# Kernel tuning notes

Measured on AMD Instinct MI355X. Metric: run time of the kernel, lower is better.

The kernel has to match this reference:

```python
import jax, jax.numpy as jnp
import numpy as np

TOP_K = 5  # top_k edges kept per node row


def _edge_update(x, w0, w1, w2, wo, bo):
    # x: [B, N, D] -> masked dense adjacency [B, N, N]
    B, N, D = x.shape
    # pairwise |x_i - x_j| then exp(-.) ; symmetric in (i, j) so the torch
    # transpose(1,3) does not change the per-pair value
    xij = jnp.exp(-jnp.abs(x[:, :, None, :] - x[:, None, :, :]))  # [B,N,N,D]
    # 1x1 convs over channel dim == einsum contractions (LeakyReLU slope 0.01)
    h = jax.nn.leaky_relu(jnp.einsum('bijd,cd->bijc', xij, w0))   # [B,N,N,2H]
    h = jax.nn.leaky_relu(jnp.einsum('bijc,oc->bijo', h, w1))     # [B,N,N,H]
    h = jax.nn.leaky_relu(jnp.einsum('bijc,oc->bijo', h, w2))     # [B,N,N,H]
    sim = jnp.einsum('bijc,oc->bijo', h, wo)[..., 0] + bo[0]      # [B,N,N]
    adj = jax.nn.sigmoid(sim) * (1.0 - jnp.eye(N, dtype=x.dtype))  # zero diag
    k = min(TOP_K, N)
    _, idx = jax.lax.top_k(adj, k)                                 # [B,N,k]
    mask = jax.nn.one_hot(idx, N, dtype=x.dtype).sum(axis=-2)      # scatter 1s
    return adj * mask, k


def _node_update(x, A, k, wn, bn, wr, br, eemb):
    # dense equivalent of PyG propagate with aggr='mean':
    # each target node t receives exactly k messages (top-k rows of A),
    # message = (neigh_x_s + edge_emb[0]) * A[t, s]
    neigh = x @ wn.T + bn                       # [B,N,D]
    e0 = eemb[0]                                # bond type 0 for graph edges
    msg = (jnp.einsum('bts,bsd->btd', A, neigh)
           + A.sum(-1, keepdims=True) * e0) / k
    return jax.nn.leaky_relu(msg + x @ wr.T + br)


def setup_inputs() -> dict:
    key = jax.random.key(0)
    n_q, n_node, d = 128, 21, 300
    H = 128
    ks = jax.random.split(key, 32)
    g = lambda i, shape, scale: (jax.random.normal(ks[i], shape, dtype=jnp.float32) * scale)
    inp = {'sample_emb': g(0, (n_q, n_node, d), 1.0)}
    i = 1
    for l in range(2):  # num_layer = 2
        inp[f'ew{l}_0'] = g(i, (2 * H, d), 0.05); i += 1
        inp[f'ew{l}_1'] = g(i, (H, 2 * H), 0.05); i += 1
        inp[f'ew{l}_2'] = g(i, (H, H), 0.05); i += 1
        inp[f'ew{l}_o'] = g(i, (1, H), 0.05); i += 1
        inp[f'eb{l}_o'] = jnp.zeros((1,), dtype=jnp.float32)
        inp[f'nw{l}_n'] = g(i, (d, d), 0.05); i += 1
        inp[f'nb{l}_n'] = jnp.zeros((d,), dtype=jnp.float32)
        inp[f'nw{l}_r'] = g(i, (d, d), 0.05); i += 1
        inp[f'nb{l}_r'] = jnp.zeros((d,), dtype=jnp.float32)
        inp[f'eemb{l}'] = g(i, (4, d), 0.1); i += 1
    return inp


def reference(sample_emb,
              ew0_0, ew0_1, ew0_2, ew0_o, eb0_o, nw0_n, nb0_n, nw0_r, nb0_r, eemb0,
              ew1_0, ew1_1, ew1_2, ew1_o, eb1_o, nw1_n, nb1_n, nw1_r, nb1_r, eemb1):
    x = sample_emb
    layers = [
        (ew0_0, ew0_1, ew0_2, ew0_o, eb0_o, nw0_n, nb0_n, nw0_r, nb0_r, eemb0),
        (ew1_0, ew1_1, ew1_2, ew1_o, eb1_o, nw1_n, nb1_n, nw1_r, nb1_r, eemb1),
    ]
    for (w0, w1, w2, wo, bo, wn, bn, wr, br, ee) in layers:
        A, k = _edge_update(x, w0, w1, w2, wo, bo)
        x = _node_update(x, A, k, wn, bn, wr, br, ee)
    return x
```

## Files before the change

kernel.cpp:

```cpp
#include <hip/hip_runtime.h>
#include <math.h>

#define B_  128
#define N_  21
#define D_  300
#define NPAIRS 231
#define NPAIR_TOT (B_ * NPAIRS)
#define GRID_E (NPAIR_TOT / 64)
#define NROWS (B_ * N_)
#define DP  320

typedef __attribute__((ext_vector_type(8))) short short8v;
typedef __attribute__((ext_vector_type(4))) float f32x4;

__device__ __forceinline__ float lrelu(float v) { return v > 0.f ? v : 0.01f * v; }

__device__ __forceinline__ unsigned short f2bf(float f) {
    unsigned u = __builtin_bit_cast(unsigned, f);
    u += 0x7FFFu + ((u >> 16) & 1u);
    return (unsigned short)(u >> 16);
}
__device__ __forceinline__ float bf2f(unsigned short h) {
    unsigned u = ((unsigned)h) << 16;
    return __builtin_bit_cast(float, u);
}

__global__ __launch_bounds__(256) void prep_all(
    const float* __restrict__ e00, const float* __restrict__ e01, const float* __restrict__ e02,
    const float* __restrict__ e10, const float* __restrict__ e11, const float* __restrict__ e12,
    const float* __restrict__ n0n, const float* __restrict__ n0r,
    const float* __restrict__ n1n, const float* __restrict__ n1r,
    unsigned short* __restrict__ ewb, unsigned short* __restrict__ nwb, int do_node)
{
    int idx = blockIdx.x * 256 + threadIdx.x;
    float v; unsigned short *ph, *pl; int off;
    if (idx < 262144) {
        int l = idx >> 17;
        int t = idx & 131071;
        unsigned short* blk = ewb + (size_t)l * 262144;
        const float* w0 = l ? e10 : e00;
        const float* w1 = l ? e11 : e01;
        const float* w2 = l ? e12 : e02;
        if (t < 81920) {
            int n = t / 320, k = t - n * 320;
            v = (k < 300) ? w0[n * 300 + k] : 0.f;
            ph = blk; pl = blk + 81920; off = t;
        } else if (t < 114688) {
            int r = t - 81920; v = w1[r];
            ph = blk + 163840; pl = blk + 196608; off = r;
        } else {
            int r = t - 114688; v = w2[r];
            ph = blk + 229376; pl = blk + 245760; off = r;
        }
    } else {
        if (!do_node) return;
        int t = idx - 262144;
        int l = t / 204800;
        int r = t - l * 204800;
        int mat = r / 102400;
        int q = r - mat * 102400;
        int n = q / 320, k = q - n * 320;
        const float* src = l ? (mat ? n1r : n1n) : (mat ? n0r : n0n);
        v = (n < 300 && k < 300) ? src[n * 300 + k] : 0.f;
        unsigned short* blk = nwb + (size_t)l * 409600;
        ph = blk + mat * 204800; pl = ph + 102400; off = q;
    }
    unsigned short hb = f2bf(v);
    ph[off] = hb; pl[off] = f2bf(v - bf2f(hb));
}

__device__ __forceinline__ short8v mk_frag(uint2 tlo, uint2 thi,
                                           int s1, int s2, bool hif)
{
    unsigned a0 = (unsigned)__shfl((int)tlo.x, s1);
    unsigned b0 = (unsigned)__shfl((int)thi.x, s1);
    unsigned a1 = (unsigned)__shfl((int)tlo.y, s1);
    unsigned b1 = (unsigned)__shfl((int)thi.y, s1);
    unsigned a2 = (unsigned)__shfl((int)tlo.x, s2);
    unsigned b2 = (unsigned)__shfl((int)thi.x, s2);
    unsigned a3 = (unsigned)__shfl((int)tlo.y, s2);
    unsigned b3 = (unsigned)__shfl((int)thi.y, s2);
    union { unsigned u[4]; short8v v; } r;
    r.u[0] = hif ? b0 : a0; r.u[1] = hif ? b1 : a1;
    r.u[2] = hif ? b2 : a2; r.u[3] = hif ? b3 : a3;
    return r.v;
}

__global__ __launch_bounds__(256, 2) void edge_mfma(
    const float* __restrict__ x,
    const unsigned short* __restrict__ w0h, const unsigned short* __restrict__ w0l,
    const unsigned short* __restrict__ w1h, const unsigned short* __restrict__ w1l,
    const unsigned short* __restrict__ w2h, const unsigned short* __restrict__ w2l,
    const float* __restrict__ wo, const float* __restrict__ bo,
    float* __restrict__ adjraw)
{
    __shared__ __align__(16) unsigned short ldsW[2][16384];

    const int tid  = threadIdx.x;
    const int lane = tid & 63;
    const int w    = tid >> 6;
    const int l15  = lane & 15;
    const int l4   = lane >> 4;

    const int p = blockIdx.x * 64 + w * 16 + l15;
    int bb = p / NPAIRS;
    int u  = p - bb * NPAIRS;
    int ii = 0;
    while (u >= N_ - ii) { u -= N_ - ii; ++ii; }
    int jj = ii + u;
    const float* xi = x + ((size_t)bb * N_ + ii) * D_;
    const float* xj = x + ((size_t)bb * N_ + jj) * D_;

    const int s1 = (lane & 15) | ((lane & 16) << 1);
    const int s2 = s1 + 16;
    const bool hif = (l4 >> 1) != 0;

    auto stage_g1 = [&](int c, int sel) {
        #pragma unroll
        for (int i = 0; i < 4; ++i) {
            const int tile = i * 4 + w;
            const size_t g = (size_t)(tile * 16 + l15) * 320 + c * 32 + l4 * 8;
            __builtin_amdgcn_global_load_lds((const unsigned int*)(w0h + g),
                (unsigned int*)(&ldsW[sel][tile * 512]), 16, 0, 0);
            __builtin_amdgcn_global_load_lds((const unsigned int*)(w0l + g),
                (unsigned int*)(&ldsW[sel][8192 + tile * 512]), 16, 0, 0);
        }
    };
    auto stage_g2 = [&](int c, int sel) {
        #pragma unroll
        for (int i = 0; i < 2; ++i) {
            const int tile = i * 4 + w;
            const size_t g = (size_t)(tile * 16 + l15) * 256 + c * 32 + l4 * 8;
            __builtin_amdgcn_global_load_lds((const unsigned int*)(w1h + g),
                (unsigned int*)(&ldsW[sel][tile * 512]), 16, 0, 0);
            __builtin_amdgcn_global_load_lds((const unsigned int*)(w1l + g),
                (unsigned int*)(&ldsW[sel][8192 + tile * 512]), 16, 0, 0);
        }
    };
    auto stage_g3 = [&](int c, int sel) {
        #pragma unroll
        for (int i = 0; i < 2; ++i) {
            const int tile = i * 4 + w;
            const size_t g = (size_t)(tile * 16 + l15) * 128 + c * 32 + l4 * 8;
            __builtin_amdgcn_global_load_lds((const unsigned int*)(w2h + g),
                (unsigned int*)(&ldsW[sel][tile * 512]), 16, 0, 0);
            __builtin_amdgcn_global_load_lds((const unsigned int*)(w2l + g),
                (unsigned int*)(&ldsW[sel][8192 + tile * 512]), 16, 0, 0);
        }
    };

    f32x4 acc[16];
    #pragma unroll
    for (int t = 0; t < 16; ++t) acc[t] = (f32x4){0.f, 0.f, 0.f, 0.f};

    stage_g1(0, 0);
    __syncthreads();

    #pragma unroll 1
    for (int c = 0; c < 10; ++c) {
        const int sel = c & 1;
        if (c < 9) stage_g1(c + 1, sel ^ 1);
        else       stage_g2(0, sel ^ 1);

        const int d0 = c * 32 + l4 * 8;
        float v[8];
        if (c < 9) {
            float4 a0 = *(const float4*)(xi + d0);
            float4 a1 = *(const float4*)(xi + d0 + 4);
            float4 b0 = *(const float4*)(xj + d0);
            float4 b1 = *(const float4*)(xj + d0 + 4);
            #pragma unroll
            for (int e = 0; e < 4; ++e) {
                v[e]     = expf(-fabsf((&a0.x)[e] - (&b0.x)[e]));
                v[4 + e] = expf(-fabsf((&a1.x)[e] - (&b1.x)[e]));
            }
        } else {
            #pragma unroll
            for (int e = 0; e < 8; ++e) {
                int d = d0 + e;
                v[e] = (d < D_) ? expf(-fabsf(xi[d] - xj[d])) : 0.f;
            }
        }
        short8v bh, bl;
        #pragma unroll
        for (int e = 0; e < 8; ++e) {
            unsigned short hb = f2bf(v[e]);
            bh[e] = (short)hb;
            bl[e] = (short)f2bf(v[e] - bf2f(hb));
        }

        #pragma unroll
        for (int t = 0; t < 16; ++t) {
            short8v wh = *(const short8v*)(&ldsW[sel][t * 512 + lane * 8]);
            short8v wl = *(const short8v*)(&ldsW[sel][8192 + t * 512 + lane * 8]);
            acc[t] = __builtin_amdgcn_mfma_f32_16x16x32_bf16(wh, bh, acc[t], 0, 0, 0);
            acc[t] = __builtin_amdgcn_mfma_f32_16x16x32_bf16(wh, bl, acc[t], 0, 0, 0);
            acc[t] = __builtin_amdgcn_mfma_f32_16x16x32_bf16(wl, bh, acc[t], 0, 0, 0);
        }
        __syncthreads();
    }

    uint2 hh[16], ll[16];
    #pragma unroll
    for (int t = 0; t < 16; ++t) {
        unsigned short h_[4], l_[4];
        #pragma unroll
        for (int r = 0; r < 4; ++r) {
            float f = lrelu(acc[t][r]);
            h_[r] = f2bf(f);
            l_[r] = f2bf(f - bf2f(h_[r]));
        }
        hh[t].x = (unsigned)h_[0] | ((unsigned)h_[1] << 16);
        hh[t].y = (unsigned)h_[2] | ((unsigned)h_[3] << 16);
        ll[t].x = (unsigned)l_[0] | ((unsigned)l_[1] << 16);
        ll[t].y = (unsigned)l_[2] | ((unsigned)l_[3] << 16);
    }

    f32x4 acc2[8];
    #pragma unroll
    for (int t = 0; t < 8; ++t) acc2[t] = (f32x4){0.f, 0.f, 0.f, 0.f};

    #pragma unroll
    for (int ks = 0; ks < 8; ++ks) {
        const int sel = ks & 1;
        if (ks < 7) stage_g2(ks + 1, sel ^ 1);
        else        stage_g3(0, sel ^ 1);

        short8v bh = mk_frag(hh[2 * ks], hh[2 * ks + 1], s1, s2, hif);
        short8v bl = mk_frag(ll[2 * ks], ll[2 * ks + 1], s1, s2, hif);

        #pragma unroll
        for (int t = 0; t < 8; ++t) {
            short8v wh = *(const short8v*)(&ldsW[sel][t * 512 + lane * 8]);
            short8v wl = *(const short8v*)(&ldsW[sel][8192 + t * 512 + lane * 8]);
            acc2[t] = __builtin_amdgcn_mfma_f32_16x16x32_bf16(wh, bh, acc2[t], 0, 0, 0);
            acc2[t] = __builtin_amdgcn_mfma_f32_16x16x32_bf16(wh, bl, acc2[t], 0, 0, 0);
            acc2[t] = __builtin_amdgcn_mfma_f32_16x16x32_bf16(wl, bh, acc2[t], 0, 0, 0);
        }
        __syncthreads();
    }

    uint2 hh1[8], ll1[8];
    #pragma unroll
    for (int t = 0; t < 8; ++t) {
        unsigned short h_[4], l_[4];
        #pragma unroll
        for (int r = 0; r < 4; ++r) {
            float f = lrelu(acc2[t][r]);
            h_[r] = f2bf(f);
            l_[r] = f2bf(f - bf2f(h_[r]));
        }
        hh1[t].x = (unsigned)h_[0] | ((unsigned)h_[1] << 16);
        hh1[t].y = (unsigned)h_[2] | ((unsigned)h_[3] << 16);
        ll1[t].x = (unsigned)l_[0] | ((unsigned)l_[1] << 16);
        ll1[t].y = (unsigned)l_[2] | ((unsigned)l_[3] << 16);
    }

    f32x4 acc3[8];
    #pragma unroll
    for (int t = 0; t < 8; ++t) acc3[t] = (f32x4){0.f, 0.f, 0.f, 0.f};

    #pragma unroll
    for (int ks = 0; ks < 4; ++ks) {
        const int sel = ks & 1;
        if (ks < 3) stage_g3(ks + 1, sel ^ 1);

        short8v bh = mk_frag(hh1[2 * ks], hh1[2 * ks + 1], s1, s2, hif);
        short8v bl = mk_frag(ll1[2 * ks], ll1[2 * ks + 1], s1, s2, hif);

        #pragma unroll
        for (int t = 0; t < 8; ++t) {
            short8v wh = *(const short8v*)(&ldsW[sel][t * 512 + lane * 8]);
            short8v wl = *(const short8v*)(&ldsW[sel][8192 + t * 512 + lane * 8]);
            acc3[t] = __builtin_amdgcn_mfma_f32_16x16x32_bf16(wh, bh, acc3[t], 0, 0, 0);
            acc3[t] = __builtin_amdgcn_mfma_f32_16x16x32_bf16(wh, bl, acc3[t], 0, 0, 0);
            acc3[t] = __builtin_amdgcn_mfma_f32_16x16x32_bf16(wl, bh, acc3[t], 0, 0, 0);
        }
        __syncthreads();
    }

    float ps = 0.f;
    #pragma unroll
    for (int t = 0; t < 8; ++t) {
        float4 wov = *(const float4*)(wo + t * 16 + l4 * 4);
        #pragma unroll
        for (int r = 0; r < 4; ++r)
            ps += lrelu(acc3[t][r]) * (&wov.x)[r];
    }
    ps += __shfl_xor(ps, 16);
    ps += __shfl_xor(ps, 32);
    if (l4 == 0) {
        float a = 1.f / (1.f + expf(-(ps + bo[0])));
        if (ii == jj) a = 0.f;
        adjraw[(size_t)bb * 441 + ii * 21 + jj] = a;
        adjraw[(size_t)bb * 441 + jj * 21 + ii] = a;
    }
}

__global__ __launch_bounds__(256, 4) void node_gemm(
    const float* __restrict__ xin,
    const unsigned short* __restrict__ wnh, const unsigned short* __restrict__ wnl,
    const unsigned short* __restrict__ wrh, const unsigned short* __restrict__ wrl,
    float* __restrict__ nbuf)
{
    __shared__ __align__(16) unsigned short sxh[2][512], sxl[2][512];

    const int tid  = threadIdx.x;
    const int lane = tid & 63;
    const int w    = tid >> 6;
    const int l15  = lane & 15;
    const int l4   = lane >> 4;
    const int M0   = blockIdx.x * 16;
    const int mat  = blockIdx.y;

    const unsigned short* ah_base = mat ? wrh : wnh;
    const unsigned short* al_base = mat ? wrl : wnl;
    float* ob = nbuf + (size_t)mat * NROWS * DP;

    const int sm = tid >> 4;
    const int sk = (tid & 15) * 2;
    const float* xrow = xin + (size_t)(M0 + sm) * D_;
    const int sa = sm * 32 + (((sk >> 3) ^ ((sm >> 1) & 3)) << 3) + (sk & 7);
    const int xr_off = l15 * 32 + ((l4 ^ ((l15 >> 1) & 3)) << 3);

    f32x4 acc[5];
    #pragma unroll
    for (int t = 0; t < 5; ++t) acc[t] = (f32x4){0.f, 0.f, 0.f, 0.f};

    {
        float2 v = *(const float2*)(xrow + sk);
        unsigned short h0 = f2bf(v.x), h1 = f2bf(v.y);
        unsigned uh = (unsigned)h0 | ((unsigned)h1 << 16);
        unsigned ul = (unsigned)f2bf(v.x - bf2f(h0)) |
                      ((unsigned)f2bf(v.y - bf2f(h1)) << 16);
        *(unsigned*)(&sxh[0][sa]) = uh;
        *(unsigned*)(&sxl[0][sa]) = ul;
    }
    __syncthreads();

    #pragma unroll 1
    for (int c = 0; c < 10; ++c) {
        const int sel = c & 1;
        short8v wh[5], wl[5];
        const int kg = c * 32 + l4 * 8;
        #pragma unroll
        for (int t = 0; t < 5; ++t) {
            const size_t n = (size_t)((w * 5 + t) * 16 + l15);
            wh[t] = *(const short8v*)(ah_base + n * DP + kg);
            wl[t] = *(const short8v*)(al_base + n * DP + kg);
        }
        float2 xv; bool have = false;
        if (c < 9) {
            const int k0 = (c + 1) * 32 + sk;
            if (k0 < D_) { xv = *(const float2*)(xrow + k0); have = true; }
        }
        short8v bh = *(const short8v*)(sxh[sel] + xr_off);
        short8v bl = *(const short8v*)(sxl[sel] + xr_off);
        #pragma unroll
        for (int t = 0; t < 5; ++t) {
            acc[t] = __builtin_amdgcn_mfma_f32_16x16x32_bf16(wh[t], bh, acc[t], 0, 0, 0);
            acc[t] = __builtin_amdgcn_mfma_f32_16x16x32_bf16(wh[t], bl, acc[t], 0, 0, 0);
            acc[t] = __builtin_amdgcn_mfma_f32_16x16x32_bf16(wl[t], bh, acc[t], 0, 0, 0);
        }
        if (c < 9) {
            unsigned uh = 0, ul = 0;
            if (have) {
                unsigned short h0 = f2bf(xv.x), h1 = f2bf(xv.y);
                uh = (unsigned)h0 | ((unsigned)h1 << 16);
                ul = (unsigned)f2bf(xv.x - bf2f(h0)) |
                     ((unsigned)f2bf(xv.y - bf2f(h1)) << 16);
            }
            *(unsigned*)(&sxh[sel ^ 1][sa]) = uh;
            *(unsigned*)(&sxl[sel ^ 1][sa]) = ul;
        }
        __syncthreads();
    }

    #pragma unroll
    for (int t = 0; t < 5; ++t) {
        const int n0 = (w * 5 + t) * 16 + l4 * 4;
        float4 v;
        v.x = acc[t][0]; v.y = acc[t][1]; v.z = acc[t][2]; v.w = acc[t][3];
        *(float4*)(ob + (size_t)(M0 + l15) * DP + n0) = v;
    }
}

__global__ __launch_bounds__(320) void node_combine(
    const float* __restrict__ adjraw, const float* __restrict__ nbuf,
    const float* __restrict__ bn, const float* __restrict__ br,
    const float* __restrict__ eemb, float* __restrict__ out)
{
    const int b = blockIdx.x;
    const int tid = threadIdx.x;
    __shared__ float sadj[N_][24];
    __shared__ float sA[N_][24];
    __shared__ float srs[N_];

    for (int it = tid; it < N_ * N_; it += 320) {
        int t = it / N_, s = it - (it / N_) * N_;
        sadj[t][s] = adjraw[(size_t)b * 441 + it];
    }
    __syncthreads();
    if (tid < N_) {
        unsigned used = 0;
        for (int r = 0; r < 5; ++r) {
            float best = -1.f; int bi = 0;
            for (int j = 0; j < N_; ++j) {
                if (used & (1u << j)) continue;
                if (sadj[tid][j] > best) { best = sadj[tid][j]; bi = j; }
            }
            used |= (1u << bi);
        }
        float rs = 0.f;
        for (int j = 0; j < N_; ++j) {
            float m = ((used >> j) & 1u) ? sadj[tid][j] : 0.f;
            sA[tid][j] = m; rs += m;
        }
        srs[tid] = rs;
    }
    __syncthreads();

    const int o = tid;
    if (o < D_) {
        const float* Pb = nbuf + (size_t)b * N_ * DP;
        const float* Rb = nbuf + (size_t)NROWS * DP + (size_t)b * N_ * DP;
        float pr[N_];
        #pragma unroll
        for (int s = 0; s < N_; ++s) pr[s] = Pb[(size_t)s * DP + o];
        const float bn_o = bn[o], br_o = br[o];
        const float add_o = bn_o + eemb[o];
        #pragma unroll
        for (int t = 0; t < N_; ++t) {
            float m = 0.f;
            #pragma unroll
            for (int s = 0; s < N_; ++s) m += sA[t][s] * pr[s];
            out[((size_t)b * N_ + t) * D_ + o] =
                lrelu((m + srs[t] * add_o) * 0.2f + Rb[(size_t)t * DP + o] + br_o);
        }
    }
}

__global__ __launch_bounds__(64) void topk_kernel(
    const float* __restrict__ adjraw, float* __restrict__ A)
{
    const int row = blockIdx.x;
    const int lane = threadIdx.x;
    __shared__ float sadj[32];
    __shared__ unsigned s_used;
    if (lane < N_) sadj[lane] = adjraw[row * N_ + lane];
    __syncthreads();
    if (lane == 0) {
        unsigned used = 0;
        for (int r = 0; r < 5; ++r) {
            float best = -1.f; int bi = 0;
            for (int j = 0; j < N_; ++j) {
                if (used & (1u << j)) continue;
                if (sadj[j] > best) { best = sadj[j]; bi = j; }
            }
            used |= (1u << bi);
        }
        s_used = used;
    }
    __syncthreads();
    if (lane < N_)
        A[row * N_ + lane] = ((s_used >> lane) & 1u) ? sadj[lane] : 0.f;
}

__global__ __launch_bounds__(320) void node_kernel(
    const float* __restrict__ xin, const float* __restrict__ A,
    const float* __restrict__ wn, const float* __restrict__ bn,
    const float* __restrict__ wr, const float* __restrict__ br,
    const float* __restrict__ eemb, float* __restrict__ out)
{
    const int b = blockIdx.x;
    const int tid = threadIdx.x;
    __shared__ float sx[N_][304];
    __shared__ float sA[N_][24];
    __shared__ float srs[N_];

    const float* xb = xin + (size_t)b * N_ * D_;
    for (int it = tid; it < N_ * D_; it += 320) {
        int j = it / D_, d = it - (it / D_) * D_;
        sx[j][d] = xb[it];
    }
    for (int it = tid; it < N_ * N_; it += 320) {
        int t = it / N_, s = it - (it / N_) * N_;
        sA[t][s] = A[((size_t)b * N_ + t) * N_ + s];
    }
    __syncthreads();
    if (tid < N_) {
        float s = 0.f;
        #pragma unroll
        for (int j = 0; j < N_; ++j) s += sA[tid][j];
        srs[tid] = s;
    }
    __syncthreads();

    const int o = tid;
    if (o < D_) {
        float nacc[N_], racc[N_];
        #pragma unroll
        for (int j = 0; j < N_; ++j) { nacc[j] = 0.f; racc[j] = 0.f; }
        const float* wnr = wn + (size_t)o * D_;
        const float* wrr = wr + (size_t)o * D_;
        for (int k4 = 0; k4 < D_; k4 += 4) {
            float4 wn4 = *(const float4*)(wnr + k4);
            float4 wr4 = *(const float4*)(wrr + k4);
            #pragma unroll
            for (int j = 0; j < N_; ++j) {
                float4 xv = *(const float4*)(&sx[j][k4]);
                nacc[j] += wn4.x * xv.x; nacc[j] += wn4.y * xv.y;
                nacc[j] += wn4.z * xv.z; nacc[j] += wn4.w * xv.w;
                racc[j] += wr4.x * xv.x; racc[j] += wr4.y * xv.y;
                racc[j] += wr4.z * xv.z; racc[j] += wr4.w * xv.w;
            }
        }
        const float bn_o = bn[o], br_o = br[o], e0_o = eemb[o];
        const float add_o = bn_o + e0_o;
        #pragma unroll
        for (int t = 0; t < N_; ++t) {
            float m = 0.f;
            #pragma unroll
            for (int s = 0; s < N_; ++s) m += sA[t][s] * nacc[s];
            out[((size_t)b * N_ + t) * D_ + o] =
                lrelu((m + srs[t] * add_o) * 0.2f + racc[t] + br_o);
        }
    }
}

extern "C" void kernel_launch(void* const* d_in, const int* in_sizes, int n_in,
                              void* d_out, int out_size, void* d_ws, size_t ws_size,
                              hipStream_t stream)
{
    const float* x0 = (const float*)d_in[0];
    auto L = [&](int l, int k) { return (const float*)d_in[1 + l * 10 + k]; };

    float* adjraw = (float*)d_ws;
    float* A      = (float*)((char*)d_ws + 262144);
    unsigned short* ewb = (unsigned short*)((char*)d_ws + 524288);
    unsigned short* nwb = (unsigned short*)((char*)d_ws + 1572864);
    float* nbuf   = (float*)((char*)d_ws + 3211264);
    const size_t WS_NEED = 10092544;
    const bool newnode = (ws_size >= WS_NEED);

    prep_all<<<2624, 256, 0, stream>>>(
        L(0,0), L(0,1), L(0,2), L(1,0), L(1,1), L(1,2),
        L(0,5), L(0,7), L(1,5), L(1,7), ewb, nwb, newnode ? 1 : 0);

    for (int l = 0; l < 2; ++l) {
        const float* xin = (l == 0) ? x0 : (const float*)d_out;
        unsigned short* blk = ewb + (size_t)l * 262144;
        edge_mfma<<<GRID_E, 256, 0, stream>>>(xin,
            blk, blk + 81920, blk + 163840, blk + 196608, blk + 229376, blk + 245760,
            L(l, 3), L(l, 4), adjraw);
        if (newnode) {
            unsigned short* nblk = nwb + (size_t)l * 409600;
            node_gemm<<<dim3(NROWS / 16, 2), 256, 0, stream>>>(
                xin, nblk, nblk + 102400, nblk + 204800, nblk + 307200, nbuf);
            node_combine<<<B_, 320, 0, stream>>>(adjraw, nbuf, L(l, 6), L(l, 8),
                                                 L(l, 9), (float*)d_out);
        } else {
            topk_kernel<<<NROWS, 64, 0, stream>>>(adjraw, A);
            node_kernel<<<B_, 320, 0, stream>>>(xin, A, L(l, 5), L(l, 6), L(l, 7),
                                                L(l, 8), L(l, 9), (float*)d_out);
        }
    }
}
```

Before: 181.0 us.

## Fuse edge MLP and node GEMM kernels into one launch with block-range dispatch

Merges the independent edge_mfma and node_gemm kernels into a single fused_en launch. Low block indices run the edge body and the rest run the node GEMM body, sharing one LDS buffer. This removes a launch and lets the two workloads run concurrently on the GPU, filling the tail of the edge grid. The node GEMM now runs under launch bounds of 2 blocks per CU and with the larger 64KB LDS allocation instead of its own smaller footprint, which lowers its occupancy.

```diff
diff --git a/kernel.cpp b/kernel.cpp
--- a/kernel.cpp
+++ b/kernel.cpp
@@ -7,6 +7,7 @@
 #define NPAIRS 231
 #define NPAIR_TOT (B_ * NPAIRS)
 #define GRID_E (NPAIR_TOT / 64)
+#define GRID_N 336
 #define NROWS (B_ * N_)
 #define DP  320
 
@@ -86,23 +87,21 @@
     return r.v;
 }
 
-__global__ __launch_bounds__(256, 2) void edge_mfma(
-    const float* __restrict__ x,
+__device__ __forceinline__ void edge_body(
+    unsigned short* lds, const float* __restrict__ x,
     const unsigned short* __restrict__ w0h, const unsigned short* __restrict__ w0l,
     const unsigned short* __restrict__ w1h, const unsigned short* __restrict__ w1l,
     const unsigned short* __restrict__ w2h, const unsigned short* __restrict__ w2l,
     const float* __restrict__ wo, const float* __restrict__ bo,
-    float* __restrict__ adjraw)
-{
-    __shared__ __align__(16) unsigned short ldsW[2][16384];
-
+    float* __restrict__ adjraw, int bid)
+{
     const int tid  = threadIdx.x;
     const int lane = tid & 63;
     const int w    = tid >> 6;
     const int l15  = lane & 15;
     const int l4   = lane >> 4;
 
-    const int p = blockIdx.x * 64 + w * 16 + l15;
+    const int p = bid * 64 + w * 16 + l15;
     int bb = p / NPAIRS;
     int u  = p - bb * NPAIRS;
     int ii = 0;
@@ -121,9 +120,9 @@
             const int tile = i * 4 + w;
             const size_t g = (size_t)(tile * 16 + l15) * 320 + c * 32 + l4 * 8;
             __builtin_amdgcn_global_load_lds((const unsigned int*)(w0h + g),
-                (unsigned int*)(&ldsW[sel][tile * 512]), 16, 0, 0);
+                (unsigned int*)(lds + sel * 16384 + tile * 512), 16, 0, 0);
             __builtin_amdgcn_global_load_lds((const unsigned int*)(w0l + g),
-                (unsigned int*)(&ldsW[sel][8192 + tile * 512]), 16, 0, 0);
+                (unsigned int*)(lds + sel * 16384 + 8192 + tile * 512), 16, 0, 0);
         }
     };
     auto stage_g2 = [&](int c, int sel) {
@@ -132,9 +131,9 @@
             const int tile = i * 4 + w;
             const size_t g = (size_t)(tile * 16 + l15) * 256 + c * 32 + l4 * 8;
             __builtin_amdgcn_global_load_lds((const unsigned int*)(w1h + g),
-                (unsigned int*)(&ldsW[sel][tile * 512]), 16, 0, 0);
+                (unsigned int*)(lds + sel * 16384 + tile * 512), 16, 0, 0);
             __builtin_amdgcn_global_load_lds((const unsigned int*)(w1l + g),
-                (unsigned int*)(&ldsW[sel][8192 + tile * 512]), 16, 0, 0);
+                (unsigned int*)(lds + sel * 16384 + 8192 + tile * 512), 16, 0, 0);
         }
     };
     auto stage_g3 = [&](int c, int sel) {
@@ -143,9 +142,9 @@
             const int tile = i * 4 + w;
             const size_t g = (size_t)(tile * 16 + l15) * 128 + c * 32 + l4 * 8;
             __builtin_amdgcn_global_load_lds((const unsigned int*)(w2h + g),
-                (unsigned int*)(&ldsW[sel][tile * 512]), 16, 0, 0);
+                (unsigned int*)(lds + sel * 16384 + tile * 512), 16, 0, 0);
             __builtin_amdgcn_global_load_lds((const unsigned int*)(w2l + g),
-                (unsigned int*)(&ldsW[sel][8192 + tile * 512]), 16, 0, 0);
+                (unsigned int*)(lds + sel * 16384 + 8192 + tile * 512), 16, 0, 0);
         }
     };
 
@@ -191,8 +190,8 @@
 
         #pragma unroll
         for (int t = 0; t < 16; ++t) {
-            short8v wh = *(const short8v*)(&ldsW[sel][t * 512 + lane * 8]);
-            short8v wl = *(const short8v*)(&ldsW[sel][8192 + t * 512 + lane * 8]);
+            short8v wh = *(const short8v*)(lds + sel * 16384 + t * 512 + lane * 8);
+            short8v wl = *(const short8v*)(lds + sel * 16384 + 8192 + t * 512 + lane * 8);
             acc[t] = __builtin_amdgcn_mfma_f32_16x16x32_bf16(wh, bh, acc[t], 0, 0, 0);
             acc[t] = __builtin_amdgcn_mfma_f32_16x16x32_bf16(wh, bl, acc[t], 0, 0, 0);
             acc[t] = __builtin_amdgcn_mfma_f32_16x16x32_bf16(wl, bh, acc[t], 0, 0, 0);
@@ -231,8 +230,8 @@
 
         #pragma unroll
         for (int t = 0; t < 8; ++t) {
-            short8v wh = *(const short8v*)(&ldsW[sel][t * 512 + lane * 8]);
-            short8v wl = *(const short8v*)(&ldsW[sel][8192 + t * 512 + lane * 8]);
+            short8v wh = *(const short8v*)(lds + sel * 16384 + t * 512 + lane * 8);
+            short8v wl = *(const short8v*)(lds + sel * 16384 + 8192 + t * 512 + lane * 8);
             acc2[t] = __builtin_amdgcn_mfma_f32_16x16x32_bf16(wh, bh, acc2[t], 0, 0, 0);
             acc2[t] = __builtin_amdgcn_mfma_f32_16x16x32_bf16(wh, bl, acc2[t], 0, 0, 0);
             acc2[t] = __builtin_amdgcn_mfma_f32_16x16x32_bf16(wl, bh, acc2[t], 0, 0, 0);
@@ -270,8 +269,8 @@
 
         #pragma unroll
         for (int t = 0; t < 8; ++t) {
-            short8v wh = *(const short8v*)(&ldsW[sel][t * 512 + lane * 8]);
-            short8v wl = *(const short8v*)(&ldsW[sel][8192 + t * 512 + lane * 8]);
+            short8v wh = *(const short8v*)(lds + sel * 16384 + t * 512 + lane * 8);
+            short8v wl = *(const short8v*)(lds + sel * 16384 + 8192 + t * 512 + lane * 8);
             acc3[t] = __builtin_amdgcn_mfma_f32_16x16x32_bf16(wh, bh, acc3[t], 0, 0, 0);
             acc3[t] = __builtin_amdgcn_mfma_f32_16x16x32_bf16(wh, bl, acc3[t], 0, 0, 0);
             acc3[t] = __builtin_amdgcn_mfma_f32_16x16x32_bf16(wl, bh, acc3[t], 0, 0, 0);
@@ -297,25 +296,18 @@
     }
 }
 
-__global__ __launch_bounds__(256, 4) void node_gemm(
-    const float* __restrict__ xin,
-    const unsigned short* __restrict__ wnh, const unsigned short* __restrict__ wnl,
-    const unsigned short* __restrict__ wrh, const unsigned short* __restrict__ wrl,
-    float* __restrict__ nbuf)
-{
-    __shared__ __align__(16) unsigned short sxh[2][512], sxl[2][512];
-
+__device__ __forceinline__ void node_body(
+    unsigned short* lds, const float* __restrict__ xin,
+    const unsigned short* __restrict__ ah_base,
+    const unsigned short* __restrict__ al_base,
+    float* __restrict__ ob, int mb)
+{
     const int tid  = threadIdx.x;
     const int lane = tid & 63;
     const int w    = tid >> 6;
     const int l15  = lane & 15;
     const int l4   = lane >> 4;
-    const int M0   = blockIdx.x * 16;
-    const int mat  = blockIdx.y;
-
-    const unsigned short* ah_base = mat ? wrh : wnh;
-    const unsigned short* al_base = mat ? wrl : wnl;
-    float* ob = nbuf + (size_t)mat * NROWS * DP;
+    const int M0   = mb * 16;
 
     const int sm = tid >> 4;
     const int sk = (tid & 15) * 2;
@@ -333,8 +325,8 @@
         unsigned uh = (unsigned)h0 | ((unsigned)h1 << 16);
         unsigned ul = (unsigned)f2bf(v.x - bf2f(h0)) |
                       ((unsigned)f2bf(v.y - bf2f(h1)) << 16);
-        *(unsigned*)(&sxh[0][sa]) = uh;
-        *(unsigned*)(&sxl[0][sa]) = ul;
+        *(unsigned*)(lds + sa) = uh;
+        *(unsigned*)(lds + 1024 + sa) = ul;
     }
     __syncthreads();
 
@@ -354,8 +346,8 @@
             const int k0 = (c + 1) * 32 + sk;
             if (k0 < D_) { xv = *(const float2*)(xrow + k0); have = true; }
         }
-        short8v bh = *(const short8v*)(sxh[sel] + xr_off);
-        short8v bl = *(const short8v*)(sxl[sel] + xr_off);
+        short8v bh = *(const short8v*)(lds + sel * 512 + xr_off);
+        short8v bl = *(const short8v*)(lds + 1024 + sel * 512 + xr_off);
         #pragma unroll
         for (int t = 0; t < 5; ++t) {
             acc[t] = __builtin_amdgcn_mfma_f32_16x16x32_bf16(wh[t], bh, acc[t], 0, 0, 0);
@@ -370,8 +362,8 @@
                 ul = (unsigned)f2bf(xv.x - bf2f(h0)) |
                      ((unsigned)f2bf(xv.y - bf2f(h1)) << 16);
             }
-            *(unsigned*)(&sxh[sel ^ 1][sa]) = uh;
-            *(unsigned*)(&sxl[sel ^ 1][sa]) = ul;
+            *(unsigned*)(lds + (sel ^ 1) * 512 + sa) = uh;
+            *(unsigned*)(lds + 1024 + (sel ^ 1) * 512 + sa) = ul;
         }
         __syncthreads();
     }
@@ -383,6 +375,39 @@
         v.x = acc[t][0]; v.y = acc[t][1]; v.z = acc[t][2]; v.w = acc[t][3];
         *(float4*)(ob + (size_t)(M0 + l15) * DP + n0) = v;
     }
+}
+
+__global__ __launch_bounds__(256, 2) void fused_en(
+    const float* __restrict__ x,
+    const unsigned short* __restrict__ ew,
+    const float* __restrict__ wo, const float* __restrict__ bo,
+    float* __restrict__ adjraw,
+    const unsigned short* __restrict__ nw,
+    float* __restrict__ nbuf)
+{
+    __shared__ __align__(16) unsigned short lds[2 * 16384];
+    if (blockIdx.x < GRID_E) {
+        edge_body(lds, x, ew, ew + 81920, ew + 163840, ew + 196608,
+                  ew + 229376, ew + 245760, wo, bo, adjraw, blockIdx.x);
+    } else {
+        const int nb = blockIdx.x - GRID_E;
+        const int mat = nb / 168;
+        const int mb  = nb - mat * 168;
+        const unsigned short* base = nw + (size_t)mat * 204800;
+        node_body(lds, x, base, base + 102400,
+                  nbuf + (size_t)mat * NROWS * DP, mb);
+    }
+}
+
+__global__ __launch_bounds__(256, 2) void edge_mfma(
+    const float* __restrict__ x,
+    const unsigned short* __restrict__ ew,
+    const float* __restrict__ wo, const float* __restrict__ bo,
+    float* __restrict__ adjraw)
+{
+    __shared__ __align__(16) unsigned short lds[2 * 16384];
+    edge_body(lds, x, ew, ew + 81920, ew + 163840, ew + 196608,
+              ew + 229376, ew + 245760, wo, bo, adjraw, blockIdx.x);
 }
 
 __global__ __launch_bounds__(320) void node_combine(
@@ -550,16 +575,14 @@
     for (int l = 0; l < 2; ++l) {
         const float* xin = (l == 0) ? x0 : (const float*)d_out;
         unsigned short* blk = ewb + (size_t)l * 262144;
-        edge_mfma<<<GRID_E, 256, 0, stream>>>(xin,
-            blk, blk + 81920, blk + 163840, blk + 196608, blk + 229376, blk + 245760,
-            L(l, 3), L(l, 4), adjraw);
         if (newnode) {
             unsigned short* nblk = nwb + (size_t)l * 409600;
-            node_gemm<<<dim3(NROWS / 16, 2), 256, 0, stream>>>(
-                xin, nblk, nblk + 102400, nblk + 204800, nblk + 307200, nbuf);
+            fused_en<<<GRID_E + GRID_N, 256, 0, stream>>>(
+                xin, blk, L(l, 3), L(l, 4), adjraw, nblk, nbuf);
             node_combine<<<B_, 320, 0, stream>>>(adjraw, nbuf, L(l, 6), L(l, 8),
                                                  L(l, 9), (float*)d_out);
         } else {
+            edge_mfma<<<GRID_E, 256, 0, stream>>>(xin, blk, L(l, 3), L(l, 4), adjraw);
             topk_kernel<<<NROWS, 64, 0, stream>>>(adjraw, A);
             node_kernel<<<B_, 320, 0, stream>>>(xin, A, L(l, 5), L(l, 6), L(l, 7),
                                                 L(l, 8), L(l, 9), (float*)d_out);
```

New measurement: 177.2 us. 2.1% less time.
